# Optimization experiments

Measured on AMD Instinct MI355X. Metric: run time of the kernel, lower is better.

The kernel has to match this reference:

```python
import jax, jax.numpy as jnp
import numpy as np

B, S_ENC, T_DEC = 32, 256, 128
E_ENC, H, E_EMB, V = 512, 512, 256, 32000


def setup_inputs() -> dict:
    key = jax.random.key(0)
    ks = jax.random.split(key, 20)
    s = 0.02
    return {
        "encoder_output": jax.random.normal(ks[0], (B, S_ENC, E_ENC), jnp.float32),
        "target_tokens": jax.random.randint(ks[1], (B, T_DEC), 0, V),
        "emb": jax.random.normal(ks[2], (V, E_EMB), jnp.float32) * s,
        # additive attention: score = v^T tanh(Wq q + bq + Wk k + bk)
        "Wq": jax.random.normal(ks[3], (H, H), jnp.float32) * s,
        "bq": jnp.zeros((H,), jnp.float32),
        "Wk": jax.random.normal(ks[4], (H, E_ENC), jnp.float32) * s,
        "bk": jnp.zeros((H,), jnp.float32),
        "v": jax.random.normal(ks[5], (H,), jnp.float32) * s,
        # 2-layer LSTM (torch gate order i,f,g,o)
        "Wih0": jax.random.normal(ks[6], (4 * H, E_EMB + E_ENC), jnp.float32) * s,
        "Whh0": jax.random.normal(ks[7], (4 * H, H), jnp.float32) * s,
        "bih0": jnp.zeros((4 * H,), jnp.float32),
        "bhh0": jnp.zeros((4 * H,), jnp.float32),
        "Wih1": jax.random.normal(ks[8], (4 * H, H), jnp.float32) * s,
        "Whh1": jax.random.normal(ks[9], (4 * H, H), jnp.float32) * s,
        "bih1": jnp.zeros((4 * H,), jnp.float32),
        "bhh1": jnp.zeros((4 * H,), jnp.float32),
        "Wout": jax.random.normal(ks[10], (V, H + E_ENC), jnp.float32) * s,
        "bout": jnp.zeros((V,), jnp.float32),
    }


def _lstm_cell(x, h, c, Wih, Whh, bih, bhh):
    g = x @ Wih.T + bih + h @ Whh.T + bhh  # (B, 4H)
    i, f, gg, o = jnp.split(g, 4, axis=-1)
    c_new = jax.nn.sigmoid(f) * c + jax.nn.sigmoid(i) * jnp.tanh(gg)
    h_new = jax.nn.sigmoid(o) * jnp.tanh(c_new)
    return h_new, c_new


def reference(encoder_output, target_tokens, emb, Wq, bq, Wk, bk, v,
              Wih0, Whh0, bih0, bhh0, Wih1, Whh1, bih1, bhh1, Wout, bout):
    hdim = Whh0.shape[1]
    bsz = encoder_output.shape[0]
    embedded = emb[target_tokens]                       # (B, T, E_emb)
    key_proj = encoder_output @ Wk.T + bk               # (B, S, H), keys fixed across steps

    def step(carry, emb_t):
        h, c = carry                                    # each (2, B, H)
        q = h[1]                                        # top-layer hidden = query
        scores = jnp.einsum("bsh,h->bs",
                            jnp.tanh(key_proj + (q @ Wq.T + bq)[:, None, :]), v)
        w = jax.nn.softmax(scores, axis=-1)             # (B, S)
        context = jnp.einsum("bs,bse->be", w, encoder_output)  # (B, E_enc)
        x0 = jnp.concatenate([emb_t, context], axis=-1)
        h0, c0 = _lstm_cell(x0, h[0], c[0], Wih0, Whh0, bih0, bhh0)
        h1, c1 = _lstm_cell(h0, h[1], c[1], Wih1, Whh1, bih1, bhh1)
        logits = jnp.concatenate([h1, context], axis=-1) @ Wout.T + bout  # (B, V)
        return (jnp.stack([h0, h1]), jnp.stack([c0, c1])), logits

    init = (jnp.zeros((2, bsz, hdim), encoder_output.dtype),
            jnp.zeros((2, bsz, hdim), encoder_output.dtype))
    (h, c), outs = jax.lax.scan(step, init, jnp.swapaxes(embedded, 0, 1))
    return jnp.swapaxes(outs, 0, 1), h, c               # (B, T, V), (2,B,H), (2,B,H)
```

## Files before the change

kernel.cpp:

```cpp
#include <hip/hip_runtime.h>
#include <hip/hip_bf16.h>

#define NB 32
#define TD 128
#define SE 256
#define HD 512
#define EEnc 512
#define EMB 256
#define NV 32000

typedef __attribute__((ext_vector_type(8))) short bf16x8;
typedef __attribute__((ext_vector_type(4))) float f32x4;

__device__ __forceinline__ float fsigm(float x){ return 1.f/(1.f+__expf(-x)); }
__device__ __forceinline__ float ftanh(float x){
  float c = fminf(fmaxf(x,-15.f),15.f);
  float e = __expf(2.f*c);
  return (e-1.f)/(e+1.f);
}


__global__ __launch_bounds__(256) void k_init(float* z){
  z[(size_t)blockIdx.x*256 + threadIdx.x] = 0.f;
}

__global__ __launch_bounds__(256) void k_gather(const float* __restrict__ emb, const int* __restrict__ tok,
                                                float* __restrict__ emb_g){
  int row = blockIdx.x;
  int tk = tok[row];
  emb_g[(size_t)row*EMB + threadIdx.x] = emb[(size_t)tk*EMB + threadIdx.x];
}

__global__ __launch_bounds__(256) void k_keyproj(const float* __restrict__ enc, const float* __restrict__ Wk,
                                                 const float* __restrict__ bk, float* __restrict__ kp){
  __shared__ float As[16][136];
  __shared__ float Bs[16*164];
  int tid = threadIdx.x;
  int bn = blockIdx.x, bm = blockIdx.y;
  int tx = tid & 15, ty = tid >> 4;
  float acc[8][8];
  #pragma unroll
  for (int i=0;i<8;i++)
    #pragma unroll
    for (int j=0;j<8;j++) acc[i][j]=0.f;
  for (int k0=0;k0<512;k0+=16){
    __syncthreads();
    #pragma unroll
    for (int r=0;r<8;r++){
      int idx = tid + r*256;
      int row = idx >> 4, kk = idx & 15;
      As[kk][row] = enc[(size_t)(bm*128+row)*EEnc + k0 + kk];
      float wv = Wk[(size_t)(bn*128+row)*EEnc + k0 + kk];
      Bs[(row>>3)*164 + kk*8 + (row&7)] = wv;
    }
    __syncthreads();
    #pragma unroll 4
    for (int kk=0;kk<16;kk++){
      float a[8], b[8];
      *(float4*)(a)   = *(float4*)&As[kk][ty*8];
      *(float4*)(a+4) = *(float4*)&As[kk][ty*8+4];
      *(float4*)(b)   = *(float4*)&Bs[tx*164 + kk*8];
      *(float4*)(b+4) = *(float4*)&Bs[tx*164 + kk*8 + 4];
      #pragma unroll
      for (int i=0;i<8;i++)
        #pragma unroll
        for (int j=0;j<8;j++) acc[i][j] += a[i]*b[j];
    }
  }
  #pragma unroll
  for (int i=0;i<8;i++){
    int row = bm*128 + ty*8 + i;
    #pragma unroll
    for (int j=0;j<8;j++){
      int col = bn*128 + tx*8 + j;
      kp[(size_t)row*HD + col] = acc[i][j] + bk[col];
    }
  }
}

__global__ __launch_bounds__(256) void k_wcat0(const float* __restrict__ Wih, const float* __restrict__ Whh,
                                               const float* __restrict__ bih, const float* __restrict__ bhh,
                                               float* __restrict__ Wcat, float* __restrict__ bcat){
  int j = blockIdx.x;
  for (int k=threadIdx.x;k<1280;k+=256){
    float v = (k<768) ? Wih[(size_t)j*768+k] : Whh[(size_t)j*512 + (k-768)];
    Wcat[(size_t)j*1280+k] = v;
  }
  if (threadIdx.x==0) bcat[j] = bih[j]+bhh[j];
}
__global__ __launch_bounds__(256) void k_wcat1(const float* __restrict__ Wih, const float* __restrict__ Whh,
                                               const float* __restrict__ bih, const float* __restrict__ bhh,
                                               float* __restrict__ Wcat, float* __restrict__ bcat){
  int j = blockIdx.x;
  for (int k=threadIdx.x;k<1024;k+=256){
    float v = (k<512) ? Wih[(size_t)j*512+k] : Whh[(size_t)j*512 + (k-512)];
    Wcat[(size_t)j*1024+k] = v;
  }
  if (threadIdx.x==0) bcat[j] = bih[j]+bhh[j];
}

__global__ __launch_bounds__(256) void k_cvtw(const float* __restrict__ W, unsigned short* __restrict__ Wb){
  size_t base = (size_t)blockIdx.x*1024 + threadIdx.x*4;
  float4 v = *(const float4*)(W + base);
  __hip_bfloat16 b0 = __float2bfloat16(v.x), b1 = __float2bfloat16(v.y);
  __hip_bfloat16 b2 = __float2bfloat16(v.z), b3 = __float2bfloat16(v.w);
  ushort4 o;
  o.x = *(unsigned short*)&b0; o.y = *(unsigned short*)&b1;
  o.z = *(unsigned short*)&b2; o.w = *(unsigned short*)&b3;
  *(ushort4*)(Wb + base) = o;
}


__global__ __launch_bounds__(256) void k_qw(const float* __restrict__ part1, const float* __restrict__ bcat1,
                                            const float* __restrict__ c1in, float* __restrict__ c1out,
                                            const float* __restrict__ Wq, const float* __restrict__ bq,
                                            float* __restrict__ qw, float* __restrict__ h1buf,
                                            __hip_bfloat16* __restrict__ X, int t){
  int hc = blockIdx.x, bg = blockIdx.y;
  int tid = threadIdx.x;
  for (int idx=tid; idx<2048; idx+=256){
    int bl = idx >> 9;
    int e  = idx & 511;
    int b  = bg*4 + bl;
    float gi = bcat1[e], gf = bcat1[512+e], gg = bcat1[1024+e], go = bcat1[1536+e];
    #pragma unroll
    for (int k2=0;k2<8;k2++){
      const float* p = part1 + (size_t)k2*65536 + (size_t)b*2048;
      gi += p[e]; gf += p[512+e]; gg += p[1024+e]; go += p[1536+e];
    }
    float cp = c1in[b*512+e];
    float cn = fsigm(gf)*cp + fsigm(gi)*ftanh(gg);
    float hn = fsigm(go)*ftanh(cn);
    c1out[b*512+e] = cn;
    h1buf[b*512+e] = hn;
    if (t > 0) X[((size_t)(b*TD + (t-1)))*1024 + e] = __float2bfloat16(hn);
  }
  __syncthreads();
  int h = hc*256 + tid;
  const float* wr = Wq + (size_t)h*HD;
  const float* x0 = h1buf + (size_t)(bg*4+0)*HD;
  const float* x1 = h1buf + (size_t)(bg*4+1)*HD;
  const float* x2 = h1buf + (size_t)(bg*4+2)*HD;
  const float* x3 = h1buf + (size_t)(bg*4+3)*HD;
  float bqh = bq[h];
  float a0=bqh, a1=bqh, a2=bqh, a3=bqh;
  #pragma unroll 4
  for (int e=0;e<HD;e+=4){
    float4 w4 = *(const float4*)(wr+e);
    float4 v0 = *(const float4*)(x0+e);
    float4 v1 = *(const float4*)(x1+e);
    float4 v2 = *(const float4*)(x2+e);
    float4 v3 = *(const float4*)(x3+e);
    a0 += w4.x*v0.x + w4.y*v0.y + w4.z*v0.z + w4.w*v0.w;
    a1 += w4.x*v1.x + w4.y*v1.y + w4.z*v1.z + w4.w*v1.w;
    a2 += w4.x*v2.x + w4.y*v2.y + w4.z*v2.z + w4.w*v2.w;
    a3 += w4.x*v3.x + w4.y*v3.y + w4.z*v3.z + w4.w*v3.w;
  }
  qw[(size_t)(bg*4+0)*HD + h] = a0;
  qw[(size_t)(bg*4+1)*HD + h] = a1;
  qw[(size_t)(bg*4+2)*HD + h] = a2;
  qw[(size_t)(bg*4+3)*HD + h] = a3;
}

__global__ __launch_bounds__(256) void k_scores(const float* __restrict__ kp, const float* __restrict__ qw,
                                                const float* __restrict__ vv, float* __restrict__ scores){
  int sc = blockIdx.x, b = blockIdx.y;
  __shared__ float qwl[512], vl[512];
  int tid = threadIdx.x;
  qwl[tid]     = qw[(size_t)b*HD + tid];
  qwl[tid+256] = qw[(size_t)b*HD + tid + 256];
  vl[tid]      = vv[tid];
  vl[tid+256]  = vv[tid+256];
  __syncthreads();
  int wave = tid>>6, lane = tid&63;
  for (int si=0; si<8; si++){
    int s = sc*32 + wave*8 + si;
    const float* row = kp + ((size_t)b*SE + s)*HD;
    float acc = 0.f;
    #pragma unroll
    for (int h=lane; h<HD; h+=64) acc += ftanh(row[h]+qwl[h]) * vl[h];
    for (int o=32;o;o>>=1) acc += __shfl_down(acc,o);
    if (lane==0) scores[b*SE+s] = acc;
  }
}

__global__ __launch_bounds__(256) void k_ctx(const float* __restrict__ scores, const float* __restrict__ enc,
                                             float* __restrict__ ctx, __hip_bfloat16* __restrict__ X, int t){
  int ec = blockIdx.x, b = blockIdx.y;
  __shared__ float w[256];
  __shared__ float red[16];
  int tid = threadIdx.x, lane = tid&63, wv = tid>>6;
  float sv = scores[b*SE + tid];
  float m = sv;
  for (int o=32;o;o>>=1) m = fmaxf(m, __shfl_down(m,o));
  if (lane==0) red[wv] = m;
  __syncthreads();
  m = fmaxf(fmaxf(red[0],red[1]),fmaxf(red[2],red[3]));
  float e = __expf(sv - m);
  w[tid] = e;
  float s = e;
  for (int o=32;o;o>>=1) s += __shfl_down(s,o);
  if (lane==0) red[4+wv] = s;
  __syncthreads();
  float inv = 1.f/(red[4]+red[5]+red[6]+red[7]);
  int e0 = ec*256 + tid;
  const float* ep = enc + (size_t)b*SE*EEnc + e0;
  float acc = 0.f;
  #pragma unroll 2
  for (int s4=0;s4<SE;s4+=4){
    float4 w4 = *(float4*)&w[s4];
    acc += w4.x*ep[(size_t)(s4  )*EEnc];
    acc += w4.y*ep[(size_t)(s4+1)*EEnc];
    acc += w4.z*ep[(size_t)(s4+2)*EEnc];
    acc += w4.w*ep[(size_t)(s4+3)*EEnc];
  }
  acc *= inv;
  ctx[(size_t)b*HD + e0] = acc;
  X[((size_t)(b*TD + t))*1024 + 512 + e0] = __float2bfloat16(acc);
}

__global__ __launch_bounds__(256) void k_g0(const float* __restrict__ Wcat0, const float* __restrict__ emb_g,
                                            const float* __restrict__ ctx, const float* __restrict__ h0buf,
                                            float* __restrict__ part0, int t){
  int ks = blockIdx.x, bg = blockIdx.y;
  int tid = threadIdx.x;
  __shared__ float xl[4][160];
  for (int idx=tid; idx<640; idx+=256){
    int bl = idx/160; int kk = idx - bl*160;
    int k = ks*160 + kk;
    int b = bg*4 + bl;
    float v;
    if (k < 256)      v = emb_g[((size_t)(b*TD + t))*EMB + k];
    else if (k < 768) v = ctx[(size_t)b*HD + (k-256)];
    else              v = h0buf[(size_t)b*HD + (k-768)];
    xl[bl][kk] = v;
  }
  __syncthreads();
  const float* wp[8];
  #pragma unroll
  for (int jj=0;jj<8;jj++) wp[jj] = Wcat0 + (size_t)(jj*256+tid)*1280 + ks*160;
  float acc[8][4];
  #pragma unroll
  for (int jj=0;jj<8;jj++){ acc[jj][0]=0.f; acc[jj][1]=0.f; acc[jj][2]=0.f; acc[jj][3]=0.f; }
  #pragma unroll 2
  for (int k=0;k<160;k+=4){
    float4 x0 = *(float4*)&xl[0][k];
    float4 x1 = *(float4*)&xl[1][k];
    float4 x2 = *(float4*)&xl[2][k];
    float4 x3 = *(float4*)&xl[3][k];
    #pragma unroll
    for (int jj=0;jj<8;jj++){
      float4 w4 = *(const float4*)(wp[jj]+k);
      acc[jj][0] += w4.x*x0.x + w4.y*x0.y + w4.z*x0.z + w4.w*x0.w;
      acc[jj][1] += w4.x*x1.x + w4.y*x1.y + w4.z*x1.z + w4.w*x1.w;
      acc[jj][2] += w4.x*x2.x + w4.y*x2.y + w4.z*x2.z + w4.w*x2.w;
      acc[jj][3] += w4.x*x3.x + w4.y*x3.y + w4.z*x3.z + w4.w*x3.w;
    }
  }
  float* pb = part0 + (size_t)ks*65536 + (size_t)(bg*4)*2048;
  #pragma unroll
  for (int jj=0;jj<8;jj++)
    #pragma unroll
    for (int bl=0;bl<4;bl++)
      pb[(size_t)bl*2048 + jj*256 + tid] = acc[jj][bl];
}

__global__ __launch_bounds__(256) void k_g1(const float* __restrict__ Wcat1, const float* __restrict__ part0,
                                            const float* __restrict__ bcat0, float* __restrict__ c0,
                                            float* __restrict__ h0buf, const float* __restrict__ h1buf,
                                            float* __restrict__ part1){
  int ks = blockIdx.x, bg = blockIdx.y;
  int tid = threadIdx.x;
  __shared__ float xl[4][128];
  if (ks < 4){
    for (int idx=tid; idx<512; idx+=256){
      int bl = idx>>7, ul = idx&127;
      int b = bg*4+bl, u = ks*128+ul;
      float gi = bcat0[u], gf = bcat0[512+u], gg = bcat0[1024+u], go = bcat0[1536+u];
      #pragma unroll
      for (int k2=0;k2<8;k2++){
        const float* p = part0 + (size_t)k2*65536 + (size_t)b*2048;
        gi += p[u]; gf += p[512+u]; gg += p[1024+u]; go += p[1536+u];
      }
      float cp = c0[(size_t)b*HD + u];
      float cn = fsigm(gf)*cp + fsigm(gi)*ftanh(gg);
      float hn = fsigm(go)*ftanh(cn);
      c0[(size_t)b*HD + u] = cn;
      h0buf[(size_t)b*HD + u] = hn;
      xl[bl][ul] = hn;
    }
  } else {
    for (int idx=tid; idx<512; idx+=256){
      int bl = idx>>7, ul = idx&127;
      xl[bl][ul] = h1buf[(size_t)(bg*4+bl)*HD + (ks-4)*128 + ul];
    }
  }
  __syncthreads();
  const float* wp[8];
  #pragma unroll
  for (int jj=0;jj<8;jj++) wp[jj] = Wcat1 + (size_t)(jj*256+tid)*1024 + ks*128;
  float acc[8][4];
  #pragma unroll
  for (int jj=0;jj<8;jj++){ acc[jj][0]=0.f; acc[jj][1]=0.f; acc[jj][2]=0.f; acc[jj][3]=0.f; }
  #pragma unroll 2
  for (int k=0;k<128;k+=4){
    float4 x0 = *(float4*)&xl[0][k];
    float4 x1 = *(float4*)&xl[1][k];
    float4 x2 = *(float4*)&xl[2][k];
    float4 x3 = *(float4*)&xl[3][k];
    #pragma unroll
    for (int jj=0;jj<8;jj++){
      float4 w4 = *(const float4*)(wp[jj]+k);
      acc[jj][0] += w4.x*x0.x + w4.y*x0.y + w4.z*x0.z + w4.w*x0.w;
      acc[jj][1] += w4.x*x1.x + w4.y*x1.y + w4.z*x1.z + w4.w*x1.w;
      acc[jj][2] += w4.x*x2.x + w4.y*x2.y + w4.z*x2.z + w4.w*x2.w;
      acc[jj][3] += w4.x*x3.x + w4.y*x3.y + w4.z*x3.z + w4.w*x3.w;
    }
  }
  float* pb = part1 + (size_t)ks*65536 + (size_t)(bg*4)*2048;
  #pragma unroll
  for (int jj=0;jj<8;jj++)
    #pragma unroll
    for (int bl=0;bl<4;bl++)
      pb[(size_t)bl*2048 + jj*256 + tid] = acc[jj][bl];
}

__global__ __launch_bounds__(256) void k_fin(const float* __restrict__ part1, const float* __restrict__ bcat1,
                                             const float* __restrict__ c1in, const float* __restrict__ h0buf,
                                             const float* __restrict__ c0, __hip_bfloat16* __restrict__ X,
                                             float* __restrict__ out){
  const size_t OUT_H = (size_t)NB*TD*NV;
  const size_t OUT_C = OUT_H + 2*NB*HD;
  int idx = blockIdx.x*256 + threadIdx.x;
  int b = idx >> 9, e = idx & 511;
  float gi = bcat1[e], gf = bcat1[512+e], gg = bcat1[1024+e], go = bcat1[1536+e];
  #pragma unroll
  for (int k2=0;k2<8;k2++){
    const float* p = part1 + (size_t)k2*65536 + (size_t)b*2048;
    gi += p[e]; gf += p[512+e]; gg += p[1024+e]; go += p[1536+e];
  }
  float cp = c1in[idx];
  float cn = fsigm(gf)*cp + fsigm(gi)*ftanh(gg);
  float hn = fsigm(go)*ftanh(cn);
  X[((size_t)(b*TD + (TD-1)))*1024 + e] = __float2bfloat16(hn);
  out[OUT_H + idx]               = h0buf[idx];
  out[OUT_H + NB*HD + idx]       = hn;
  out[OUT_C + idx]               = c0[idx];
  out[OUT_C + NB*HD + idx]       = cn;
}

__global__ __launch_bounds__(256) void k_gemm(const unsigned short* __restrict__ X,
                                              const unsigned short* __restrict__ W,
                                              const float* __restrict__ bout, float* __restrict__ out){
  __shared__ unsigned short As[128][64];
  __shared__ unsigned short Bs[128][64];
  int tid = threadIdx.x;
  int bn = blockIdx.x, bm = blockIdx.y;
  int wave = tid>>6, lane = tid&63;
  int wm = wave&1, wn = wave>>1;
  int r16 = lane&15, quad = lane>>4;
  f32x4 acc[4][4];
  #pragma unroll
  for (int i=0;i<4;i++)
    #pragma unroll
    for (int j=0;j<4;j++){ f32x4 z = {0.f,0.f,0.f,0.f}; acc[i][j] = z; }
  for (int k0=0;k0<1024;k0+=64){
    __syncthreads();
    #pragma unroll
    for (int i=0;i<4;i++){
      int idx = tid + i*256;
      int row = idx>>3, ch = idx&7;
      int sw = ch ^ (row&7);
      *(uint4*)&As[row][sw*8] = *(const uint4*)(X + (size_t)(bm*128+row)*1024 + k0 + ch*8);
      *(uint4*)&Bs[row][sw*8] = *(const uint4*)(W + (size_t)(bn*128+row)*1024 + k0 + ch*8);
    }
    __syncthreads();
    #pragma unroll
    for (int kk=0;kk<2;kk++){
      bf16x8 af[4], bf[4];
      #pragma unroll
      for (int i=0;i<4;i++){
        int ar = wm*64 + i*16 + r16;
        int ach = (kk*4 + quad) ^ (ar&7);
        af[i] = *(bf16x8*)&As[ar][ach*8];
        int br = wn*64 + i*16 + r16;
        int bch = (kk*4 + quad) ^ (br&7);
        bf[i] = *(bf16x8*)&Bs[br][bch*8];
      }
      #pragma unroll
      for (int i=0;i<4;i++)
        #pragma unroll
        for (int j=0;j<4;j++)
          acc[i][j] = __builtin_amdgcn_mfma_f32_16x16x32_bf16(af[i], bf[j], acc[i][j], 0,0,0);
    }
  }
  #pragma unroll
  for (int j=0;j<4;j++){
    int col = bn*128 + wn*64 + j*16 + r16;
    float bo = bout[col];
    #pragma unroll
    for (int i=0;i<4;i++){
      int row0 = bm*128 + wm*64 + i*16 + quad*4;
      #pragma unroll
      for (int r=0;r<4;r++)
        out[(size_t)(row0+r)*NV + col] = acc[i][j][r] + bo;
    }
  }
}


extern "C" void kernel_launch(void* const* d_in, const int* in_sizes, int n_in,
                              void* d_out, int out_size, void* d_ws, size_t ws_size,
                              hipStream_t stream){
  (void)in_sizes; (void)n_in; (void)out_size; (void)ws_size;
  const float* enc  = (const float*)d_in[0];
  const int*   tok  = (const int*)d_in[1];
  const float* emb  = (const float*)d_in[2];
  const float* Wq   = (const float*)d_in[3];
  const float* bq   = (const float*)d_in[4];
  const float* Wk   = (const float*)d_in[5];
  const float* bk   = (const float*)d_in[6];
  const float* vv   = (const float*)d_in[7];
  const float* Wih0 = (const float*)d_in[8];
  const float* Whh0 = (const float*)d_in[9];
  const float* bih0 = (const float*)d_in[10];
  const float* bhh0 = (const float*)d_in[11];
  const float* Wih1 = (const float*)d_in[12];
  const float* Whh1 = (const float*)d_in[13];
  const float* bih1 = (const float*)d_in[14];
  const float* bhh1 = (const float*)d_in[15];
  const float* Wout = (const float*)d_in[16];
  const float* bout = (const float*)d_in[17];
  float* out = (float*)d_out;

  float* wsf = (float*)d_ws;
  float* kp    = wsf + 0;
  float* emb_g = wsf + 4194304;
  float* qw    = wsf + 5242880;
  float* scores= wsf + 5259264;
  float* ctx   = wsf + 5267456;
  float* h1buf = wsf + 5283840;
  float* c1b   = wsf + 5300224;
  float* h0buf = wsf + 5316608;
  float* c0    = wsf + 5332992;
  float* c1a   = wsf + 5349376;
  float* part1 = wsf + 5365760;
  float* part0 = wsf + 5890048;
  float* Wcat0 = wsf + 6414336;
  float* Wcat1 = wsf + 9035776;
  float* bcat0 = wsf + 11132928;
  float* bcat1 = wsf + 11134976;
  char* wsb = (char*)d_ws;
  __hip_bfloat16* X = (__hip_bfloat16*)(wsb + 44548096);
  unsigned short* Woutb = (unsigned short*)(wsb + 52936704);

  hipLaunchKernelGGL(k_init,   dim3(2240), dim3(256), 0, stream, h0buf);
  hipLaunchKernelGGL(k_gather, dim3(NB*TD), dim3(256), 0, stream, emb, tok, emb_g);
  hipLaunchKernelGGL(k_keyproj,dim3(4,64), dim3(256), 0, stream, enc, Wk, bk, kp);
  hipLaunchKernelGGL(k_wcat0,  dim3(2048), dim3(256), 0, stream, Wih0, Whh0, bih0, bhh0, Wcat0, bcat0);
  hipLaunchKernelGGL(k_wcat1,  dim3(2048), dim3(256), 0, stream, Wih1, Whh1, bih1, bhh1, Wcat1, bcat1);
  hipLaunchKernelGGL(k_cvtw,   dim3(NV),   dim3(256), 0, stream, Wout, Woutb);

  for (int t=0; t<TD; t++){
    float* c1in  = (t&1) ? c1b : c1a;
    float* c1out = (t&1) ? c1a : c1b;
    hipLaunchKernelGGL(k_qw,     dim3(2,8),  dim3(256), 0, stream,
                       part1, bcat1, c1in, c1out, Wq, bq, qw, h1buf, X, t);
    hipLaunchKernelGGL(k_scores, dim3(8,NB), dim3(256), 0, stream, kp, qw, vv, scores);
    hipLaunchKernelGGL(k_ctx,    dim3(2,NB), dim3(256), 0, stream, scores, enc, ctx, X, t);
    hipLaunchKernelGGL(k_g0,     dim3(8,8),  dim3(256), 0, stream, Wcat0, emb_g, ctx, h0buf, part0, t);
    hipLaunchKernelGGL(k_g1,     dim3(8,8),  dim3(256), 0, stream, Wcat1, part0, bcat0, c0, h0buf, h1buf, part1);
  }
  hipLaunchKernelGGL(k_fin,  dim3(64), dim3(256), 0, stream, part1, bcat1, c1a, h0buf, c0, X, out);
  hipLaunchKernelGGL(k_gemm, dim3(NV/128, (NB*TD)/128), dim3(256), 0, stream,
                     (const unsigned short*)X, Woutb, bout, out);
}
```

Measured before the change: 19.84 ms.

## Fuse recurrent decoder loop into one persistent kernel with group grid barriers

Replaces the 640 per-timestep kernel launches with a single persistent kernel of 256 blocks. The blocks are split into 4 independent groups of 64, each owning 8 batch rows, and the phases inside a step are separated by software grid barriers built on atomics. The LSTM weights are reordered so gates are interleaved per hidden unit, which lets one block finish a full cell update without split-K partial buffers. Wq is pre-transposed. This removes launch overhead and the partial-sum round trips through global memory. In exchange it depends on all 256 blocks being co-resident, and spin barriers add latency.

```diff
diff --git a/kernel.cpp b/kernel.cpp
--- a/kernel.cpp
+++ b/kernel.cpp
@@ -18,6 +18,7 @@
   float e = __expf(2.f*c);
   return (e-1.f)/(e+1.f);
 }
+
 
 
 __global__ __launch_bounds__(256) void k_init(float* z){
@@ -80,23 +81,34 @@
 
 __global__ __launch_bounds__(256) void k_wcat0(const float* __restrict__ Wih, const float* __restrict__ Whh,
                                                const float* __restrict__ bih, const float* __restrict__ bhh,
-                                               float* __restrict__ Wcat, float* __restrict__ bcat){
+                                               float* __restrict__ Wi, float* __restrict__ bi){
   int j = blockIdx.x;
+  int jr = (j & 511)*4 + (j >> 9);
   for (int k=threadIdx.x;k<1280;k+=256){
     float v = (k<768) ? Wih[(size_t)j*768+k] : Whh[(size_t)j*512 + (k-768)];
-    Wcat[(size_t)j*1280+k] = v;
-  }
-  if (threadIdx.x==0) bcat[j] = bih[j]+bhh[j];
+    Wi[(size_t)jr*1280+k] = v;
+  }
+  if (threadIdx.x==0) bi[jr] = bih[j]+bhh[j];
 }
 __global__ __launch_bounds__(256) void k_wcat1(const float* __restrict__ Wih, const float* __restrict__ Whh,
                                                const float* __restrict__ bih, const float* __restrict__ bhh,
-                                               float* __restrict__ Wcat, float* __restrict__ bcat){
+                                               float* __restrict__ Wi, float* __restrict__ bi){
   int j = blockIdx.x;
+  int jr = (j & 511)*4 + (j >> 9);
   for (int k=threadIdx.x;k<1024;k+=256){
     float v = (k<512) ? Wih[(size_t)j*512+k] : Whh[(size_t)j*512 + (k-512)];
-    Wcat[(size_t)j*1024+k] = v;
-  }
-  if (threadIdx.x==0) bcat[j] = bih[j]+bhh[j];
+    Wi[(size_t)jr*1024+k] = v;
+  }
+  if (threadIdx.x==0) bi[jr] = bih[j]+bhh[j];
+}
+
+__global__ __launch_bounds__(256) void k_trq(const float* __restrict__ W, float* __restrict__ WT){
+  __shared__ float t[32][33];
+  int h0 = blockIdx.x*32, e0 = blockIdx.y*32;
+  int x = threadIdx.x & 31, y = threadIdx.x >> 5;
+  for (int r=y; r<32; r+=8) t[r][x] = W[(size_t)(h0+r)*512 + e0+x];
+  __syncthreads();
+  for (int r=y; r<32; r+=8) WT[(size_t)(e0+r)*512 + h0+x] = t[x][r];
 }
 
 __global__ __launch_bounds__(256) void k_cvtw(const float* __restrict__ W, unsigned short* __restrict__ Wb){
@@ -111,242 +123,264 @@
 }
 
 
-__global__ __launch_bounds__(256) void k_qw(const float* __restrict__ part1, const float* __restrict__ bcat1,
-                                            const float* __restrict__ c1in, float* __restrict__ c1out,
-                                            const float* __restrict__ Wq, const float* __restrict__ bq,
-                                            float* __restrict__ qw, float* __restrict__ h1buf,
-                                            __hip_bfloat16* __restrict__ X, int t){
-  int hc = blockIdx.x, bg = blockIdx.y;
-  int tid = threadIdx.x;
-  for (int idx=tid; idx<2048; idx+=256){
-    int bl = idx >> 9;
-    int e  = idx & 511;
-    int b  = bg*4 + bl;
-    float gi = bcat1[e], gf = bcat1[512+e], gg = bcat1[1024+e], go = bcat1[1536+e];
-    #pragma unroll
-    for (int k2=0;k2<8;k2++){
-      const float* p = part1 + (size_t)k2*65536 + (size_t)b*2048;
-      gi += p[e]; gf += p[512+e]; gg += p[1024+e]; go += p[1536+e];
-    }
-    float cp = c1in[b*512+e];
-    float cn = fsigm(gf)*cp + fsigm(gi)*ftanh(gg);
-    float hn = fsigm(go)*ftanh(cn);
-    c1out[b*512+e] = cn;
-    h1buf[b*512+e] = hn;
-    if (t > 0) X[((size_t)(b*TD + (t-1)))*1024 + e] = __float2bfloat16(hn);
-  }
+__device__ __forceinline__ void gbar(unsigned* bar, int lb, unsigned &sense){
   __syncthreads();
-  int h = hc*256 + tid;
-  const float* wr = Wq + (size_t)h*HD;
-  const float* x0 = h1buf + (size_t)(bg*4+0)*HD;
-  const float* x1 = h1buf + (size_t)(bg*4+1)*HD;
-  const float* x2 = h1buf + (size_t)(bg*4+2)*HD;
-  const float* x3 = h1buf + (size_t)(bg*4+3)*HD;
-  float bqh = bq[h];
-  float a0=bqh, a1=bqh, a2=bqh, a3=bqh;
-  #pragma unroll 4
-  for (int e=0;e<HD;e+=4){
-    float4 w4 = *(const float4*)(wr+e);
-    float4 v0 = *(const float4*)(x0+e);
-    float4 v1 = *(const float4*)(x1+e);
-    float4 v2 = *(const float4*)(x2+e);
-    float4 v3 = *(const float4*)(x3+e);
-    a0 += w4.x*v0.x + w4.y*v0.y + w4.z*v0.z + w4.w*v0.w;
-    a1 += w4.x*v1.x + w4.y*v1.y + w4.z*v1.z + w4.w*v1.w;
-    a2 += w4.x*v2.x + w4.y*v2.y + w4.z*v2.z + w4.w*v2.w;
-    a3 += w4.x*v3.x + w4.y*v3.y + w4.z*v3.z + w4.w*v3.w;
-  }
-  qw[(size_t)(bg*4+0)*HD + h] = a0;
-  qw[(size_t)(bg*4+1)*HD + h] = a1;
-  qw[(size_t)(bg*4+2)*HD + h] = a2;
-  qw[(size_t)(bg*4+3)*HD + h] = a3;
-}
-
-__global__ __launch_bounds__(256) void k_scores(const float* __restrict__ kp, const float* __restrict__ qw,
-                                                const float* __restrict__ vv, float* __restrict__ scores){
-  int sc = blockIdx.x, b = blockIdx.y;
-  __shared__ float qwl[512], vl[512];
-  int tid = threadIdx.x;
-  qwl[tid]     = qw[(size_t)b*HD + tid];
-  qwl[tid+256] = qw[(size_t)b*HD + tid + 256];
-  vl[tid]      = vv[tid];
-  vl[tid+256]  = vv[tid+256];
+  if (threadIdx.x == 0){
+    sense ^= 1u;
+    __threadfence();
+    unsigned* subc = bar + 16 + (lb >> 3)*16;
+    unsigned p = __hip_atomic_fetch_add(subc, 1u, __ATOMIC_ACQ_REL, __HIP_MEMORY_SCOPE_AGENT);
+    if (p == 7u){
+      __hip_atomic_store(subc, 0u, __ATOMIC_RELAXED, __HIP_MEMORY_SCOPE_AGENT);
+      unsigned q = __hip_atomic_fetch_add(bar, 1u, __ATOMIC_ACQ_REL, __HIP_MEMORY_SCOPE_AGENT);
+      if (q == 7u){
+        __hip_atomic_store(bar, 0u, __ATOMIC_RELAXED, __HIP_MEMORY_SCOPE_AGENT);
+        __hip_atomic_store(bar + 1, sense, __ATOMIC_RELEASE, __HIP_MEMORY_SCOPE_AGENT);
+      }
+    }
+    while (__hip_atomic_load(bar + 1, __ATOMIC_ACQUIRE, __HIP_MEMORY_SCOPE_AGENT) != sense)
+      __builtin_amdgcn_s_sleep(2);
+    __threadfence();
+  }
   __syncthreads();
-  int wave = tid>>6, lane = tid&63;
-  for (int si=0; si<8; si++){
-    int s = sc*32 + wave*8 + si;
-    const float* row = kp + ((size_t)b*SE + s)*HD;
-    float acc = 0.f;
-    #pragma unroll
-    for (int h=lane; h<HD; h+=64) acc += ftanh(row[h]+qwl[h]) * vl[h];
-    for (int o=32;o;o>>=1) acc += __shfl_down(acc,o);
-    if (lane==0) scores[b*SE+s] = acc;
-  }
-}
-
-__global__ __launch_bounds__(256) void k_ctx(const float* __restrict__ scores, const float* __restrict__ enc,
-                                             float* __restrict__ ctx, __hip_bfloat16* __restrict__ X, int t){
-  int ec = blockIdx.x, b = blockIdx.y;
-  __shared__ float w[256];
-  __shared__ float red[16];
-  int tid = threadIdx.x, lane = tid&63, wv = tid>>6;
-  float sv = scores[b*SE + tid];
-  float m = sv;
-  for (int o=32;o;o>>=1) m = fmaxf(m, __shfl_down(m,o));
-  if (lane==0) red[wv] = m;
-  __syncthreads();
-  m = fmaxf(fmaxf(red[0],red[1]),fmaxf(red[2],red[3]));
-  float e = __expf(sv - m);
-  w[tid] = e;
-  float s = e;
-  for (int o=32;o;o>>=1) s += __shfl_down(s,o);
-  if (lane==0) red[4+wv] = s;
-  __syncthreads();
-  float inv = 1.f/(red[4]+red[5]+red[6]+red[7]);
-  int e0 = ec*256 + tid;
-  const float* ep = enc + (size_t)b*SE*EEnc + e0;
-  float acc = 0.f;
-  #pragma unroll 2
-  for (int s4=0;s4<SE;s4+=4){
-    float4 w4 = *(float4*)&w[s4];
-    acc += w4.x*ep[(size_t)(s4  )*EEnc];
-    acc += w4.y*ep[(size_t)(s4+1)*EEnc];
-    acc += w4.z*ep[(size_t)(s4+2)*EEnc];
-    acc += w4.w*ep[(size_t)(s4+3)*EEnc];
-  }
-  acc *= inv;
-  ctx[(size_t)b*HD + e0] = acc;
-  X[((size_t)(b*TD + t))*1024 + 512 + e0] = __float2bfloat16(acc);
-}
-
-__global__ __launch_bounds__(256) void k_g0(const float* __restrict__ Wcat0, const float* __restrict__ emb_g,
-                                            const float* __restrict__ ctx, const float* __restrict__ h0buf,
-                                            float* __restrict__ part0, int t){
-  int ks = blockIdx.x, bg = blockIdx.y;
-  int tid = threadIdx.x;
-  __shared__ float xl[4][160];
-  for (int idx=tid; idx<640; idx+=256){
-    int bl = idx/160; int kk = idx - bl*160;
-    int k = ks*160 + kk;
-    int b = bg*4 + bl;
-    float v;
-    if (k < 256)      v = emb_g[((size_t)(b*TD + t))*EMB + k];
-    else if (k < 768) v = ctx[(size_t)b*HD + (k-256)];
-    else              v = h0buf[(size_t)b*HD + (k-768)];
-    xl[bl][kk] = v;
-  }
-  __syncthreads();
-  const float* wp[8];
-  #pragma unroll
-  for (int jj=0;jj<8;jj++) wp[jj] = Wcat0 + (size_t)(jj*256+tid)*1280 + ks*160;
-  float acc[8][4];
-  #pragma unroll
-  for (int jj=0;jj<8;jj++){ acc[jj][0]=0.f; acc[jj][1]=0.f; acc[jj][2]=0.f; acc[jj][3]=0.f; }
-  #pragma unroll 2
-  for (int k=0;k<160;k+=4){
-    float4 x0 = *(float4*)&xl[0][k];
-    float4 x1 = *(float4*)&xl[1][k];
-    float4 x2 = *(float4*)&xl[2][k];
-    float4 x3 = *(float4*)&xl[3][k];
-    #pragma unroll
-    for (int jj=0;jj<8;jj++){
-      float4 w4 = *(const float4*)(wp[jj]+k);
-      acc[jj][0] += w4.x*x0.x + w4.y*x0.y + w4.z*x0.z + w4.w*x0.w;
-      acc[jj][1] += w4.x*x1.x + w4.y*x1.y + w4.z*x1.z + w4.w*x1.w;
-      acc[jj][2] += w4.x*x2.x + w4.y*x2.y + w4.z*x2.z + w4.w*x2.w;
-      acc[jj][3] += w4.x*x3.x + w4.y*x3.y + w4.z*x3.z + w4.w*x3.w;
-    }
-  }
-  float* pb = part0 + (size_t)ks*65536 + (size_t)(bg*4)*2048;
-  #pragma unroll
-  for (int jj=0;jj<8;jj++)
-    #pragma unroll
-    for (int bl=0;bl<4;bl++)
-      pb[(size_t)bl*2048 + jj*256 + tid] = acc[jj][bl];
-}
-
-__global__ __launch_bounds__(256) void k_g1(const float* __restrict__ Wcat1, const float* __restrict__ part0,
-                                            const float* __restrict__ bcat0, float* __restrict__ c0,
-                                            float* __restrict__ h0buf, const float* __restrict__ h1buf,
-                                            float* __restrict__ part1){
-  int ks = blockIdx.x, bg = blockIdx.y;
-  int tid = threadIdx.x;
-  __shared__ float xl[4][128];
-  if (ks < 4){
-    for (int idx=tid; idx<512; idx+=256){
-      int bl = idx>>7, ul = idx&127;
-      int b = bg*4+bl, u = ks*128+ul;
-      float gi = bcat0[u], gf = bcat0[512+u], gg = bcat0[1024+u], go = bcat0[1536+u];
-      #pragma unroll
-      for (int k2=0;k2<8;k2++){
-        const float* p = part0 + (size_t)k2*65536 + (size_t)b*2048;
-        gi += p[u]; gf += p[512+u]; gg += p[1024+u]; go += p[1536+u];
-      }
-      float cp = c0[(size_t)b*HD + u];
-      float cn = fsigm(gf)*cp + fsigm(gi)*ftanh(gg);
-      float hn = fsigm(go)*ftanh(cn);
-      c0[(size_t)b*HD + u] = cn;
-      h0buf[(size_t)b*HD + u] = hn;
-      xl[bl][ul] = hn;
-    }
-  } else {
-    for (int idx=tid; idx<512; idx+=256){
-      int bl = idx>>7, ul = idx&127;
-      xl[bl][ul] = h1buf[(size_t)(bg*4+bl)*HD + (ks-4)*128 + ul];
-    }
-  }
-  __syncthreads();
-  const float* wp[8];
-  #pragma unroll
-  for (int jj=0;jj<8;jj++) wp[jj] = Wcat1 + (size_t)(jj*256+tid)*1024 + ks*128;
-  float acc[8][4];
-  #pragma unroll
-  for (int jj=0;jj<8;jj++){ acc[jj][0]=0.f; acc[jj][1]=0.f; acc[jj][2]=0.f; acc[jj][3]=0.f; }
-  #pragma unroll 2
-  for (int k=0;k<128;k+=4){
-    float4 x0 = *(float4*)&xl[0][k];
-    float4 x1 = *(float4*)&xl[1][k];
-    float4 x2 = *(float4*)&xl[2][k];
-    float4 x3 = *(float4*)&xl[3][k];
-    #pragma unroll
-    for (int jj=0;jj<8;jj++){
-      float4 w4 = *(const float4*)(wp[jj]+k);
-      acc[jj][0] += w4.x*x0.x + w4.y*x0.y + w4.z*x0.z + w4.w*x0.w;
-      acc[jj][1] += w4.x*x1.x + w4.y*x1.y + w4.z*x1.z + w4.w*x1.w;
-      acc[jj][2] += w4.x*x2.x + w4.y*x2.y + w4.z*x2.z + w4.w*x2.w;
-      acc[jj][3] += w4.x*x3.x + w4.y*x3.y + w4.z*x3.z + w4.w*x3.w;
-    }
-  }
-  float* pb = part1 + (size_t)ks*65536 + (size_t)(bg*4)*2048;
-  #pragma unroll
-  for (int jj=0;jj<8;jj++)
-    #pragma unroll
-    for (int bl=0;bl<4;bl++)
-      pb[(size_t)bl*2048 + jj*256 + tid] = acc[jj][bl];
-}
-
-__global__ __launch_bounds__(256) void k_fin(const float* __restrict__ part1, const float* __restrict__ bcat1,
-                                             const float* __restrict__ c1in, const float* __restrict__ h0buf,
-                                             const float* __restrict__ c0, __hip_bfloat16* __restrict__ X,
-                                             float* __restrict__ out){
-  const size_t OUT_H = (size_t)NB*TD*NV;
-  const size_t OUT_C = OUT_H + 2*NB*HD;
-  int idx = blockIdx.x*256 + threadIdx.x;
-  int b = idx >> 9, e = idx & 511;
-  float gi = bcat1[e], gf = bcat1[512+e], gg = bcat1[1024+e], go = bcat1[1536+e];
-  #pragma unroll
-  for (int k2=0;k2<8;k2++){
-    const float* p = part1 + (size_t)k2*65536 + (size_t)b*2048;
-    gi += p[e]; gf += p[512+e]; gg += p[1024+e]; go += p[1536+e];
-  }
-  float cp = c1in[idx];
-  float cn = fsigm(gf)*cp + fsigm(gi)*ftanh(gg);
-  float hn = fsigm(go)*ftanh(cn);
-  X[((size_t)(b*TD + (TD-1)))*1024 + e] = __float2bfloat16(hn);
-  out[OUT_H + idx]               = h0buf[idx];
-  out[OUT_H + NB*HD + idx]       = hn;
-  out[OUT_C + idx]               = c0[idx];
-  out[OUT_C + NB*HD + idx]       = cn;
+}
+
+__global__ __launch_bounds__(256) void k_step(const float* __restrict__ enc,
+                                              const float* __restrict__ bq,
+                                              const float* __restrict__ vv,
+                                              float* __restrict__ wsf,
+                                              float* __restrict__ out){
+  const float* kp    = wsf;
+  const float* emb_g = wsf + 4194304;
+  float* qw     = wsf + 5242880;
+  float* scores = wsf + 5259264;
+  float* ctx    = wsf + 5267456;
+  float* h0pp   = wsf + 5283840;
+  float* h1pp   = wsf + 5316608;
+  float* c0     = wsf + 5349376;
+  float* c1     = wsf + 5365760;
+  unsigned* bars= (unsigned*)(wsf + 5382144);
+  const float* WqT = wsf + 5383168;
+  const float* Wi0 = wsf + 5645312;
+  const float* Wi1 = wsf + 8266752;
+  const float* bi0 = wsf + 10363904;
+  const float* bi1 = wsf + 10365952;
+  __hip_bfloat16* X = (__hip_bfloat16*)((char*)wsf + 44548096);
+
+  const int gid = blockIdx.x;
+  const int grp = gid >> 6;
+  const int lb  = gid & 63;
+  const int tid = threadIdx.x;
+  unsigned* bar = bars + grp*256;
+  unsigned sense = 0;
+
+  __shared__ __align__(16) float xs[10240];
+  __shared__ __align__(16) float red[2176];
+  __shared__ __align__(16) float aux[1088];
+
+  for (int t=0; t<TD; t++){
+    const int p = t & 1;
+    const float* h1p = h1pp + p*16384;
+    float*       h1n = h1pp + (p^1)*16384;
+    const float* h0p = h0pp + p*16384;
+    float*       h0n = h0pp + (p^1)*16384;
+
+    {
+      #pragma unroll
+      for (int bL=0; bL<8; bL++){
+        int bb = grp*8 + bL;
+        for (int e=tid; e<HD; e+=256) xs[bL*520 + e] = h1p[(size_t)bb*HD + e];
+      }
+      __syncthreads();
+      int hL = tid & 7, sp = tid >> 3;
+      const float* wp = WqT + (size_t)(sp*16)*HD + lb*8 + hL;
+      float a[8];
+      #pragma unroll
+      for (int i=0;i<8;i++) a[i]=0.f;
+      #pragma unroll
+      for (int e=0;e<16;e++){
+        float w = wp[(size_t)e*HD];
+        #pragma unroll
+        for (int bL=0;bL<8;bL++) a[bL] += w * xs[bL*520 + sp*16 + e];
+      }
+      #pragma unroll
+      for (int bL=0;bL<8;bL++) red[(hL*8+bL)*34 + sp] = a[bL];
+      __syncthreads();
+      if (tid < 64){
+        int hL2 = tid >> 3, bL2 = tid & 7;
+        const float* pr = red + (hL2*8+bL2)*34;
+        float s = bq[lb*8 + hL2];
+        #pragma unroll
+        for (int q2=0;q2<32;q2++) s += pr[q2];
+        qw[(size_t)(grp*8+bL2)*HD + lb*8 + hL2] = s;
+      }
+    }
+    gbar(bar, lb, sense);
+
+    {
+      int sc = lb >> 3;
+      int bb = grp*8 + (lb & 7);
+      aux[tid]       = qw[(size_t)bb*HD + tid];
+      aux[tid + 256] = qw[(size_t)bb*HD + tid + 256];
+      aux[tid + 512] = vv[tid];
+      aux[tid + 768] = vv[tid + 256];
+      __syncthreads();
+      int lane = tid & 63, wv = tid >> 6;
+      #pragma unroll
+      for (int si=0; si<8; si++){
+        int s = sc*32 + wv*8 + si;
+        const float* row = kp + ((size_t)bb*SE + s)*HD;
+        float acc = 0.f;
+        #pragma unroll
+        for (int i=0;i<8;i++){
+          int h = lane + i*64;
+          acc += ftanh(row[h] + aux[h]) * aux[512 + h];
+        }
+        for (int o=32;o;o>>=1) acc += __shfl_down(acc, o);
+        if (lane==0) scores[(size_t)bb*SE + s] = acc;
+      }
+    }
+    gbar(bar, lb, sense);
+
+    {
+      int ec = lb >> 3;
+      int bb = grp*8 + (lb & 7);
+      int lane = tid & 63, wv = tid >> 6;
+      float sv = scores[(size_t)bb*SE + tid];
+      float m = sv;
+      for (int o=32;o;o>>=1) m = fmaxf(m, __shfl_xor(m, o));
+      if (lane==0) red[wv] = m;
+      __syncthreads();
+      m = fmaxf(fmaxf(red[0],red[1]), fmaxf(red[2],red[3]));
+      float ex = __expf(sv - m);
+      aux[tid] = ex;
+      float sum = ex;
+      for (int o=32;o;o>>=1) sum += __shfl_xor(sum, o);
+      if (lane==0) red[8+wv] = sum;
+      __syncthreads();
+      float inv = 1.f/(red[8]+red[9]+red[10]+red[11]);
+      const float* ep = enc + ((size_t)bb*SE + wv*64)*EEnc + ec*64 + lane;
+      const float* wl = aux + wv*64;
+      float acc = 0.f;
+      #pragma unroll 4
+      for (int s=0;s<64;s++) acc += wl[s] * ep[(size_t)s*EEnc];
+      red[16 + wv*64 + lane] = acc;
+      __syncthreads();
+      if (tid < 64){
+        float c = (red[16+tid]+red[80+tid]+red[144+tid]+red[208+tid]) * inv;
+        ctx[(size_t)bb*HD + ec*64 + tid] = c;
+        X[((size_t)bb*TD + t)*1024 + 512 + ec*64 + tid] = __float2bfloat16(c);
+      }
+    }
+    gbar(bar, lb, sense);
+
+    {
+      #pragma unroll
+      for (int bL=0; bL<8; bL++){
+        int bb = grp*8 + bL;
+        for (int k=tid; k<1280; k+=256){
+          float v;
+          if (k < 256)      v = emb_g[((size_t)bb*TD + t)*EMB + k];
+          else if (k < 768) v = ctx[(size_t)bb*HD + (k-256)];
+          else              v = h0p[(size_t)bb*HD + (k-768)];
+          xs[bL*1280 + k] = v;
+        }
+      }
+      __syncthreads();
+      int r = tid & 31, kq = tid >> 5;
+      const float* wrow = Wi0 + (size_t)(lb*32 + r)*1280 + kq*160;
+      float a[8];
+      #pragma unroll
+      for (int i=0;i<8;i++) a[i]=0.f;
+      #pragma unroll 2
+      for (int k=0;k<160;k+=4){
+        float4 w4 = *(const float4*)(wrow + k);
+        #pragma unroll
+        for (int bL=0;bL<8;bL++){
+          float4 x4 = *(const float4*)&xs[bL*1280 + kq*160 + k];
+          a[bL] += w4.x*x4.x + w4.y*x4.y + w4.z*x4.z + w4.w*x4.w;
+        }
+      }
+      #pragma unroll
+      for (int bL=0;bL<8;bL++) red[(bL*8+kq)*34 + r] = a[bL];
+      __syncthreads();
+      if (tid < 64){
+        int uL = tid >> 3, bL = tid & 7;
+        int u = lb*8 + uL, bb = grp*8 + bL;
+        float gi = bi0[u*4+0], gf = bi0[u*4+1], gg = bi0[u*4+2], go = bi0[u*4+3];
+        #pragma unroll
+        for (int q=0;q<8;q++){
+          const float* pr = red + (bL*8+q)*34 + uL*4;
+          gi += pr[0]; gf += pr[1]; gg += pr[2]; go += pr[3];
+        }
+        float cp = c0[(size_t)bb*HD + u];
+        float cn = fsigm(gf)*cp + fsigm(gi)*ftanh(gg);
+        float hn = fsigm(go)*ftanh(cn);
+        c0[(size_t)bb*HD + u] = cn;
+        h0n[(size_t)bb*HD + u] = hn;
+      }
+    }
+    gbar(bar, lb, sense);
+
+    {
+      #pragma unroll
+      for (int bL=0; bL<8; bL++){
+        int bb = grp*8 + bL;
+        for (int k=tid; k<1024; k+=256){
+          float v = (k < 512) ? h0n[(size_t)bb*HD + k] : h1p[(size_t)bb*HD + (k-512)];
+          xs[bL*1024 + k] = v;
+        }
+      }
+      __syncthreads();
+      int r = tid & 31, kq = tid >> 5;
+      const float* wrow = Wi1 + (size_t)(lb*32 + r)*1024 + kq*128;
+      float a[8];
+      #pragma unroll
+      for (int i=0;i<8;i++) a[i]=0.f;
+      #pragma unroll 2
+      for (int k=0;k<128;k+=4){
+        float4 w4 = *(const float4*)(wrow + k);
+        #pragma unroll
+        for (int bL=0;bL<8;bL++){
+          float4 x4 = *(const float4*)&xs[bL*1024 + kq*128 + k];
+          a[bL] += w4.x*x4.x + w4.y*x4.y + w4.z*x4.z + w4.w*x4.w;
+        }
+      }
+      #pragma unroll
+      for (int bL=0;bL<8;bL++) red[(bL*8+kq)*34 + r] = a[bL];
+      __syncthreads();
+      if (tid < 64){
+        int uL = tid >> 3, bL = tid & 7;
+        int u = lb*8 + uL, bb = grp*8 + bL;
+        float gi = bi1[u*4+0], gf = bi1[u*4+1], gg = bi1[u*4+2], go = bi1[u*4+3];
+        #pragma unroll
+        for (int q=0;q<8;q++){
+          const float* pr = red + (bL*8+q)*34 + uL*4;
+          gi += pr[0]; gf += pr[1]; gg += pr[2]; go += pr[3];
+        }
+        float cp = c1[(size_t)bb*HD + u];
+        float cn = fsigm(gf)*cp + fsigm(gi)*ftanh(gg);
+        float hn = fsigm(go)*ftanh(cn);
+        c1[(size_t)bb*HD + u] = cn;
+        h1n[(size_t)bb*HD + u] = hn;
+        X[((size_t)bb*TD + t)*1024 + u] = __float2bfloat16(hn);
+      }
+    }
+    gbar(bar, lb, sense);
+  }
+
+  if (lb < 8){
+    int bb = grp*8 + lb;
+    const size_t OUT_H = (size_t)NB*TD*NV;
+    const size_t OUT_C = OUT_H + (size_t)2*NB*HD;
+    for (int e=tid; e<HD; e+=256){
+      size_t base = (size_t)bb*HD + e;
+      out[OUT_H + base]                 = h0pp[base];
+      out[OUT_H + (size_t)NB*HD + base] = h1pp[base];
+      out[OUT_C + base]                 = c0[base];
+      out[OUT_C + (size_t)NB*HD + base] = c1[base];
+    }
+  }
 }
 
 __global__ __launch_bounds__(256) void k_gemm(const unsigned short* __restrict__ X,
@@ -436,42 +470,25 @@
   float* wsf = (float*)d_ws;
   float* kp    = wsf + 0;
   float* emb_g = wsf + 4194304;
-  float* qw    = wsf + 5242880;
-  float* scores= wsf + 5259264;
-  float* ctx   = wsf + 5267456;
-  float* h1buf = wsf + 5283840;
-  float* c1b   = wsf + 5300224;
-  float* h0buf = wsf + 5316608;
-  float* c0    = wsf + 5332992;
-  float* c1a   = wsf + 5349376;
-  float* part1 = wsf + 5365760;
-  float* part0 = wsf + 5890048;
-  float* Wcat0 = wsf + 6414336;
-  float* Wcat1 = wsf + 9035776;
-  float* bcat0 = wsf + 11132928;
-  float* bcat1 = wsf + 11134976;
+  float* WqT   = wsf + 5383168;
+  float* Wi0   = wsf + 5645312;
+  float* Wi1   = wsf + 8266752;
+  float* bi0   = wsf + 10363904;
+  float* bi1   = wsf + 10365952;
   char* wsb = (char*)d_ws;
   __hip_bfloat16* X = (__hip_bfloat16*)(wsb + 44548096);
   unsigned short* Woutb = (unsigned short*)(wsb + 52936704);
 
-  hipLaunchKernelGGL(k_init,   dim3(2240), dim3(256), 0, stream, h0buf);
-  hipLaunchKernelGGL(k_gather, dim3(NB*TD), dim3(256), 0, stream, emb, tok, emb_g);
+  hipLaunchKernelGGL(k_init,   dim3(388),  dim3(256), 0, stream, wsf + 5283840);
+  hipLaunchKernelGGL(k_gather, dim3(NB*TD),dim3(256), 0, stream, emb, tok, emb_g);
   hipLaunchKernelGGL(k_keyproj,dim3(4,64), dim3(256), 0, stream, enc, Wk, bk, kp);
-  hipLaunchKernelGGL(k_wcat0,  dim3(2048), dim3(256), 0, stream, Wih0, Whh0, bih0, bhh0, Wcat0, bcat0);
-  hipLaunchKernelGGL(k_wcat1,  dim3(2048), dim3(256), 0, stream, Wih1, Whh1, bih1, bhh1, Wcat1, bcat1);
+  hipLaunchKernelGGL(k_wcat0,  dim3(2048), dim3(256), 0, stream, Wih0, Whh0, bih0, bhh0, Wi0, bi0);
+  hipLaunchKernelGGL(k_wcat1,  dim3(2048), dim3(256), 0, stream, Wih1, Whh1, bih1, bhh1, Wi1, bi1);
+  hipLaunchKernelGGL(k_trq,    dim3(16,16),dim3(256), 0, stream, Wq, WqT);
   hipLaunchKernelGGL(k_cvtw,   dim3(NV),   dim3(256), 0, stream, Wout, Woutb);
 
-  for (int t=0; t<TD; t++){
-    float* c1in  = (t&1) ? c1b : c1a;
-    float* c1out = (t&1) ? c1a : c1b;
-    hipLaunchKernelGGL(k_qw,     dim3(2,8),  dim3(256), 0, stream,
-                       part1, bcat1, c1in, c1out, Wq, bq, qw, h1buf, X, t);
-    hipLaunchKernelGGL(k_scores, dim3(8,NB), dim3(256), 0, stream, kp, qw, vv, scores);
-    hipLaunchKernelGGL(k_ctx,    dim3(2,NB), dim3(256), 0, stream, scores, enc, ctx, X, t);
-    hipLaunchKernelGGL(k_g0,     dim3(8,8),  dim3(256), 0, stream, Wcat0, emb_g, ctx, h0buf, part0, t);
-    hipLaunchKernelGGL(k_g1,     dim3(8,8),  dim3(256), 0, stream, Wcat1, part0, bcat0, c0, h0buf, h1buf, part1);
-  }
-  hipLaunchKernelGGL(k_fin,  dim3(64), dim3(256), 0, stream, part1, bcat1, c1a, h0buf, c0, X, out);
+  hipLaunchKernelGGL(k_step, dim3(256), dim3(256), 0, stream, enc, bq, vv, wsf, out);
+
   hipLaunchKernelGGL(k_gemm, dim3(NV/128, (NB*TD)/128), dim3(256), 0, stream,
                      (const unsigned short*)X, Woutb, bout, out);
 }
```

Result: slower. 26.15 ms (+31.8%).
